# Kernel optimization log

Measured on AMD Instinct MI355X. Metric: run time of the kernel, lower is better.

The kernel has to match this reference:

```python
import jax, jax.numpy as jnp
import numpy as np

NUM_EXPERTS = 8
TOPK = 2
INPUT_DIM = 2048
OUTPUT_DIM = 2048


def setup_inputs() -> dict:
    key = jax.random.key(0)
    k_x, k_w, k_gw, k_gb = jax.random.split(key, 4)
    x = jax.random.normal(k_x, (8192, INPUT_DIM), dtype=jnp.float32)
    # experts: Linear(input_dim, output_dim*num_experts), xavier_uniform weight, zero bias
    fan_out = OUTPUT_DIM * NUM_EXPERTS
    limit = float(np.sqrt(6.0 / (INPUT_DIM + fan_out)))
    expert_w = jax.random.uniform(k_w, (fan_out, INPUT_DIM), minval=-limit, maxval=limit, dtype=jnp.float32)
    expert_b = jnp.zeros((fan_out,), dtype=jnp.float32)
    # gate: Linear(input_dim, num_experts), default torch init (uniform +-1/sqrt(fan_in))
    gl = 1.0 / float(np.sqrt(INPUT_DIM))
    gate_w = jax.random.uniform(k_gw, (NUM_EXPERTS, INPUT_DIM), minval=-gl, maxval=gl, dtype=jnp.float32)
    gate_b = jax.random.uniform(k_gb, (NUM_EXPERTS,), minval=-gl, maxval=gl, dtype=jnp.float32)
    return {"x": x, "expert_w": expert_w, "expert_b": expert_b, "gate_w": gate_w, "gate_b": gate_b}


def reference(x, expert_w, expert_b, gate_w, gate_b):
    B = x.shape[0]
    # gating
    gate_logits = x @ gate_w.T + gate_b                      # [B, E]
    gate_probs = jax.nn.softmax(gate_logits, axis=-1)
    top_k_probs, top_k_idx = jax.lax.top_k(gate_probs, TOPK)  # [B, K]
    # dense expert GEMM: all experts computed
    expert_out = x @ expert_w.T + expert_b                   # [B, E*D_out]
    expert_out = expert_out.reshape(B, NUM_EXPERTS, OUTPUT_DIM)
    # gather selected experts per token and combine
    sel = jnp.take_along_axis(expert_out, top_k_idx[:, :, None], axis=1)  # [B, K, D_out]
    out = jnp.sum(sel * top_k_probs[:, :, None], axis=1)     # [B, D_out]
    return out
```

## Files before the change

kernel.cpp:

```cpp
#include <hip/hip_runtime.h>

#define NUM_TOKENS 8192
#define DIM 2048
#define NE 8
#define BM 128
#define BN 128
#define BK 64

typedef __bf16 bf16x8 __attribute__((ext_vector_type(8)));
typedef float f32x4 __attribute__((ext_vector_type(4)));

typedef __attribute__((address_space(1))) const void* as1_cvp;
typedef __attribute__((address_space(3))) void* as3_vp;

__device__ __forceinline__ unsigned short f2bf(float f) {
  unsigned int u = __float_as_uint(f);
  unsigned int lsb = (u >> 16) & 1u;
  u += 0x7fffu + lsb;
  return (unsigned short)(u >> 16);
}
__device__ __forceinline__ float bflo(unsigned int u) {
  return __uint_as_float(u << 16);
}
__device__ __forceinline__ float bfhi(unsigned int u) {
  return __uint_as_float(u & 0xffff0000u);
}

__global__ __launch_bounds__(256) void convert_w_kernel(
    const float4* __restrict__ w, ushort4* __restrict__ wb) {
  int i = blockIdx.x * 256 + threadIdx.x;
  float4 v = w[i];
  ushort4 o;
  o.x = f2bf(v.x); o.y = f2bf(v.y); o.z = f2bf(v.z); o.w = f2bf(v.w);
  wb[i] = o;
}

__global__ __launch_bounds__(256) void gating_kernel(
    const float* __restrict__ x, const float* __restrict__ gw,
    const float* __restrict__ gb, unsigned short* __restrict__ xb,
    float* __restrict__ probs, int* __restrict__ routed) {
  const int wave = threadIdx.x >> 6;
  const int lane = threadIdx.x & 63;
  const int t = blockIdx.x * 4 + wave;
  const float4* xrow = (const float4*)(x + (size_t)t * DIM);
  ushort4* xbrow = (ushort4*)(xb + (size_t)t * DIM);
  float acc[NE];
#pragma unroll
  for (int e = 0; e < NE; ++e) acc[e] = 0.f;
#pragma unroll
  for (int it = 0; it < DIM / (4 * 64); ++it) {
    const int k4 = it * 64 + lane;
    float4 xv = xrow[k4];
    ushort4 o;
    o.x = f2bf(xv.x); o.y = f2bf(xv.y); o.z = f2bf(xv.z); o.w = f2bf(xv.w);
    xbrow[k4] = o;
#pragma unroll
    for (int e = 0; e < NE; ++e) {
      float4 wv = ((const float4*)(gw + (size_t)e * DIM))[k4];
      acc[e] += xv.x * wv.x + xv.y * wv.y + xv.z * wv.z + xv.w * wv.w;
    }
  }
#pragma unroll
  for (int e = 0; e < NE; ++e) {
#pragma unroll
    for (int off = 32; off > 0; off >>= 1)
      acc[e] += __shfl_xor(acc[e], off, 64);
  }
  if (lane == 0) {
    float p[NE];
    float mx = -1e30f;
#pragma unroll
    for (int e = 0; e < NE; ++e) {
      p[e] = acc[e] + gb[e];
      mx = fmaxf(mx, p[e]);
    }
    float s = 0.f;
#pragma unroll
    for (int e = 0; e < NE; ++e) { p[e] = __expf(p[e] - mx); s += p[e]; }
    float inv = 1.f / s;
#pragma unroll
    for (int e = 0; e < NE; ++e) p[e] *= inv;
    int e0 = 0;
#pragma unroll
    for (int e = 1; e < NE; ++e) if (p[e] > p[e0]) e0 = e;
    int e1 = (e0 == 0) ? 1 : 0;
#pragma unroll
    for (int e = 0; e < NE; ++e) if (e != e0 && p[e] > p[e1]) e1 = e;
    probs[t * 2 + 0] = p[e0];
    probs[t * 2 + 1] = p[e1];
    routed[t] = e0 | (e1 << 8);
  }
}

__global__ __launch_bounds__(256) void build_lists_kernel(
    const int* __restrict__ routed, int* __restrict__ lists,
    int* __restrict__ counts, int* __restrict__ tokpos) {
  const int e = blockIdx.x;
  const int tid = threadIdx.x;
  __shared__ int sc[256];
  __shared__ int sb[256];
  const int base_t = tid * (NUM_TOKENS / 256);
  int c = 0, cb = 0;
#pragma unroll 4
  for (int j = 0; j < NUM_TOKENS / 256; ++j) {
    int r = routed[base_t + j];
    int a0 = r & 0xff, a1 = (r >> 8) & 0xff;
    c += (a0 == e) + (a1 == e);
    cb += (a0 < e) + (a1 < e);
  }
  sc[tid] = c;
  sb[tid] = cb;
  __syncthreads();
  for (int ofs = 1; ofs < 256; ofs <<= 1) {
    int v = (tid >= ofs) ? sc[tid - ofs] : 0;
    int w = (tid >= ofs) ? sb[tid - ofs] : 0;
    __syncthreads();
    sc[tid] += v;
    sb[tid] += w;
    __syncthreads();
  }
  const int ebase = sb[255];
  int pos = sc[tid] - c;
#pragma unroll 4
  for (int j = 0; j < NUM_TOKENS / 256; ++j) {
    int t = base_t + j;
    int r = routed[t];
    if ((r & 0xff) == e) {
      lists[e * NUM_TOKENS + pos] = t;
      tokpos[2 * t] = ebase + pos;
      pos++;
    }
    if (((r >> 8) & 0xff) == e) {
      lists[e * NUM_TOKENS + pos] = t | 0x10000;
      tokpos[2 * t + 1] = ebase + pos;
      pos++;
    }
  }
  if (tid == 255) {
    counts[e] = sc[255];
    counts[8 + e] = ebase;
  }
}

__global__ __launch_bounds__(256) void moe_gemm_kernel(
    const unsigned short* __restrict__ xb,
    const unsigned short* __restrict__ wb,
    const float* __restrict__ eb,
    const float* __restrict__ probs,
    const int* __restrict__ lists,
    const int* __restrict__ counts,
    unsigned short* __restrict__ y,
    float* __restrict__ out,
    int use_y) {
  const int e = blockIdx.z;
  const int cnt = counts[e];
  const int s = blockIdx.x + 16 * blockIdx.y;
  const int xcd = s & 7;
  const int j = s >> 3;
  const int R = (j >> 4) * 8 + xcd;
  const int w4 = j & 15;
  const int mt = (R >> 2) * 4 + (w4 & 3);
  const int nt = (R & 3) * 4 + (w4 >> 2);
  const int m0 = mt * BM;
  if (m0 >= cnt) return;
  const int n0 = nt * BN;

  __shared__ __attribute__((aligned(16))) unsigned short As[BM * BK];
  __shared__ __attribute__((aligned(16))) unsigned short Bs[BN * BK];

  const int tid = threadIdx.x;
  const int wave = tid >> 6;
  const int lane = tid & 63;
  const int srow = lane >> 3;
  const int scol = ((lane & 7) ^ srow) * 8;

  const unsigned short* ag[4];
  const unsigned short* bg[4];
#pragma unroll
  for (int i = 0; i < 4; ++i) {
    int r = m0 + wave * 32 + i * 8 + srow;
    int rc = r < cnt ? r : cnt - 1;
    int tok = lists[e * NUM_TOKENS + rc] & 0xFFFF;
    ag[i] = xb + (size_t)tok * DIM + scol;
    int wr = e * DIM + n0 + wave * 32 + i * 8 + srow;
    bg[i] = wb + (size_t)wr * DIM + scol;
  }

  const f32x4 zero = {0.f, 0.f, 0.f, 0.f};
  f32x4 acc[4][4];
#pragma unroll
  for (int a = 0; a < 4; ++a)
#pragma unroll
    for (int b = 0; b < 4; ++b) acc[a][b] = zero;

  const int wm = (wave >> 1) * 64;
  const int wn = (wave & 1) * 64;
  const int frow = lane & 15;
  const int csel = lane >> 4;
  const int swz = lane & 7;

  for (int k0 = 0; k0 < DIM; k0 += BK) {
    __syncthreads();
#pragma unroll
    for (int i = 0; i < 4; ++i) {
      __builtin_amdgcn_global_load_lds(
          (as1_cvp)(ag[i] + k0),
          (as3_vp)(As + (wave * 32 + i * 8) * BK), 16, 0, 0);
      __builtin_amdgcn_global_load_lds(
          (as1_cvp)(bg[i] + k0),
          (as3_vp)(Bs + (wave * 32 + i * 8) * BK), 16, 0, 0);
    }
    __syncthreads();
#pragma unroll
    for (int kk = 0; kk < BK; kk += 32) {
      const int koff = ((((kk >> 3) | csel) ^ swz) << 3);
      bf16x8 af[4], bfr[4];
#pragma unroll
      for (int im = 0; im < 4; ++im)
        af[im] = *(const bf16x8*)(As + (wm + im * 16 + frow) * BK + koff);
#pragma unroll
      for (int in_ = 0; in_ < 4; ++in_)
        bfr[in_] = *(const bf16x8*)(Bs + (wn + in_ * 16 + frow) * BK + koff);
#pragma unroll
      for (int im = 0; im < 4; ++im)
#pragma unroll
        for (int in_ = 0; in_ < 4; ++in_)
          acc[im][in_] = __builtin_amdgcn_mfma_f32_16x16x32_bf16(
              af[im], bfr[in_], acc[im][in_], 0, 0, 0);
    }
  }

  const int quad = lane >> 4;
  const int col = lane & 15;
  const int ybase = counts[8 + e];
#pragma unroll
  for (int im = 0; im < 4; ++im) {
#pragma unroll
    for (int reg = 0; reg < 4; ++reg) {
      int r = m0 + wm + im * 16 + quad * 4 + reg;
      if (r >= cnt) continue;
      if (use_y) {
        unsigned short* yrow = y + (size_t)(ybase + r) * DIM;
#pragma unroll
        for (int in_ = 0; in_ < 4; ++in_) {
          int n = n0 + wn + in_ * 16 + col;
          yrow[n] = f2bf(acc[im][in_][reg] + eb[e * DIM + n]);
        }
      } else {
        int entry = lists[e * NUM_TOKENS + r];
        int tok = entry & 0xFFFF;
        int slot = entry >> 16;
        float p = probs[tok * 2 + slot];
        float* orow = out + (size_t)tok * DIM;
#pragma unroll
        for (int in_ = 0; in_ < 4; ++in_) {
          int n = n0 + wn + in_ * 16 + col;
          float v = acc[im][in_][reg] + eb[e * DIM + n];
          atomicAdd(orow + n, p * v);
        }
      }
    }
  }
}

__global__ __launch_bounds__(256) void combine_kernel(
    const unsigned short* __restrict__ y, const float* __restrict__ probs,
    const int* __restrict__ tokpos, float* __restrict__ out) {
  const int t = blockIdx.x;
  const int tid = threadIdx.x;
  const int i0 = tokpos[2 * t], i1 = tokpos[2 * t + 1];
  const float p0 = probs[2 * t], p1 = probs[2 * t + 1];
  uint4 a = ((const uint4*)(y + (size_t)i0 * DIM))[tid];
  uint4 b = ((const uint4*)(y + (size_t)i1 * DIM))[tid];
  float4 o0, o1;
  o0.x = p0 * bflo(a.x) + p1 * bflo(b.x);
  o0.y = p0 * bfhi(a.x) + p1 * bfhi(b.x);
  o0.z = p0 * bflo(a.y) + p1 * bflo(b.y);
  o0.w = p0 * bfhi(a.y) + p1 * bfhi(b.y);
  o1.x = p0 * bflo(a.z) + p1 * bflo(b.z);
  o1.y = p0 * bfhi(a.z) + p1 * bfhi(b.z);
  o1.z = p0 * bflo(a.w) + p1 * bflo(b.w);
  o1.w = p0 * bfhi(a.w) + p1 * bfhi(b.w);
  float4* orow = (float4*)(out + (size_t)t * DIM);
  orow[2 * tid] = o0;
  orow[2 * tid + 1] = o1;
}

extern "C" void kernel_launch(void* const* d_in, const int* in_sizes, int n_in,
                              void* d_out, int out_size, void* d_ws, size_t ws_size,
                              hipStream_t stream) {
  const float* x  = (const float*)d_in[0];
  const float* ew = (const float*)d_in[1];
  const float* eb = (const float*)d_in[2];
  const float* gw = (const float*)d_in[3];
  const float* gb = (const float*)d_in[4];
  float* out = (float*)d_out;
  char* p = (char*)d_ws;

  const size_t NEED = 67108864ull + 33554432ull + 67108864ull + 65536ull +
                      262144ull + 64ull + 32768ull + 65536ull;
  const int use_y = (ws_size >= NEED) ? 1 : 0;

  unsigned short* wb = (unsigned short*)p; p += 67108864;
  unsigned short* xb = (unsigned short*)p; p += 33554432;
  unsigned short* y = nullptr;
  if (use_y) { y = (unsigned short*)p; p += 67108864; }
  float* probs = (float*)p; p += 65536;
  int* lists   = (int*)p;   p += 262144;
  int* counts  = (int*)p;   p += 64;
  int* routed  = (int*)p;   p += 32768;
  int* tokpos  = (int*)p;   p += 65536;

  if (!use_y)
    hipMemsetAsync(out, 0, (size_t)NUM_TOKENS * DIM * sizeof(float), stream);
  convert_w_kernel<<<(NE * DIM * DIM / 4) / 256, 256, 0, stream>>>(
      (const float4*)ew, (ushort4*)wb);
  gating_kernel<<<NUM_TOKENS / 4, 256, 0, stream>>>(x, gw, gb, xb, probs,
                                                    routed);
  build_lists_kernel<<<NE, 256, 0, stream>>>(routed, lists, counts, tokpos);
  moe_gemm_kernel<<<dim3(DIM / BN, NUM_TOKENS / BM, NE), 256, 0, stream>>>(
      xb, wb, eb, probs, lists, counts, y, out, use_y);
  if (use_y)
    combine_kernel<<<NUM_TOKENS, 256, 0, stream>>>(y, probs, tokpos, out);
}
```

Before: 505.5 us.

## Enlarge MoE GEMM tiles to 256x256 with double-buffered LDS pipeline

Rewrites the grouped expert GEMM to use 256x256 tiles with 512 threads (8 waves, each computing 128x64), double-buffered LDS, and prefetch of the next K tile via direct global-to-LDS loads interleaved between MFMA phases. It also uses s_setprio around MFMA bursts and explicit vmcnt waits with raw barriers. The XCD-aware tile remapping is dropped in favour of plain block indexing. This is meant to raise arithmetic intensity and hide global-load latency, at the cost of 128 KB of LDS per block, more registers, and coarser tiles that waste more work on partially filled expert row tiles.

```diff
diff --git a/kernel.cpp b/kernel.cpp
--- a/kernel.cpp
+++ b/kernel.cpp
@@ -3,9 +3,10 @@
 #define NUM_TOKENS 8192
 #define DIM 2048
 #define NE 8
-#define BM 128
-#define BN 128
+#define BM 256
+#define BN 256
 #define BK 64
+#define KTILES (DIM / BK)
 
 typedef __bf16 bf16x8 __attribute__((ext_vector_type(8)));
 typedef float f32x4 __attribute__((ext_vector_type(4)));
@@ -25,6 +26,8 @@
 __device__ __forceinline__ float bfhi(unsigned int u) {
   return __uint_as_float(u & 0xffff0000u);
 }
+
+#define CFENCE() asm volatile("" ::: "memory")
 
 __global__ __launch_bounds__(256) void convert_w_kernel(
     const float4* __restrict__ w, ushort4* __restrict__ wb) {
@@ -142,7 +145,7 @@
   }
 }
 
-__global__ __launch_bounds__(256) void moe_gemm_kernel(
+__global__ __launch_bounds__(512, 2) void moe_gemm_kernel(
     const unsigned short* __restrict__ xb,
     const unsigned short* __restrict__ wb,
     const float* __restrict__ eb,
@@ -154,109 +157,171 @@
     int use_y) {
   const int e = blockIdx.z;
   const int cnt = counts[e];
-  const int s = blockIdx.x + 16 * blockIdx.y;
-  const int xcd = s & 7;
-  const int j = s >> 3;
-  const int R = (j >> 4) * 8 + xcd;
-  const int w4 = j & 15;
-  const int mt = (R >> 2) * 4 + (w4 & 3);
-  const int nt = (R & 3) * 4 + (w4 >> 2);
-  const int m0 = mt * BM;
+  const int m0 = blockIdx.y * BM;
   if (m0 >= cnt) return;
-  const int n0 = nt * BN;
-
-  __shared__ __attribute__((aligned(16))) unsigned short As[BM * BK];
-  __shared__ __attribute__((aligned(16))) unsigned short Bs[BN * BK];
+  const int n0 = blockIdx.x * BN;
+
+  __shared__ __attribute__((aligned(16))) unsigned short As[2][BM * BK];
+  __shared__ __attribute__((aligned(16))) unsigned short Bs[2][BN * BK];
 
   const int tid = threadIdx.x;
-  const int wave = tid >> 6;
-  const int lane = tid & 63;
-  const int srow = lane >> 3;
-  const int scol = ((lane & 7) ^ srow) * 8;
-
-  const unsigned short* ag[4];
-  const unsigned short* bg[4];
-#pragma unroll
-  for (int i = 0; i < 4; ++i) {
-    int r = m0 + wave * 32 + i * 8 + srow;
+  const int w = tid >> 6;
+  const int ln = tid & 63;
+  const int sr8 = ln >> 3;
+  const int sgc = ((ln & 7) ^ sr8) * 8;
+
+  const unsigned short* asrc[4];
+  const unsigned short* bsrc[4];
+#pragma unroll
+  for (int rb = 0; rb < 4; ++rb) {
+    int r = m0 + rb * 64 + w * 8 + sr8;
     int rc = r < cnt ? r : cnt - 1;
     int tok = lists[e * NUM_TOKENS + rc] & 0xFFFF;
-    ag[i] = xb + (size_t)tok * DIM + scol;
-    int wr = e * DIM + n0 + wave * 32 + i * 8 + srow;
-    bg[i] = wb + (size_t)wr * DIM + scol;
-  }
+    asrc[rb] = xb + (size_t)tok * DIM + sgc;
+    int wr = e * DIM + n0 + rb * 64 + w * 8 + sr8;
+    bsrc[rb] = wb + (size_t)wr * DIM + sgc;
+  }
+
+#define STAGE_A(buf, rb, k0)                                      \
+  __builtin_amdgcn_global_load_lds(                               \
+      (as1_cvp)(asrc[rb] + (k0)),                                 \
+      (as3_vp)(&As[buf][((rb)*64 + w * 8) * 64]), 16, 0, 0)
+#define STAGE_B(buf, rb, k0)                                      \
+  __builtin_amdgcn_global_load_lds(                               \
+      (as1_cvp)(bsrc[rb] + (k0)),                                 \
+      (as3_vp)(&Bs[buf][((rb)*64 + w * 8) * 64]), 16, 0, 0)
+
+#define BAR()            \
+  do {                   \
+    CFENCE();            \
+    __builtin_amdgcn_s_barrier(); \
+    CFENCE();            \
+  } while (0)
 
   const f32x4 zero = {0.f, 0.f, 0.f, 0.f};
-  f32x4 acc[4][4];
-#pragma unroll
-  for (int a = 0; a < 4; ++a)
+  f32x4 acc[8][4];
+#pragma unroll
+  for (int a = 0; a < 8; ++a)
 #pragma unroll
     for (int b = 0; b < 4; ++b) acc[a][b] = zero;
 
-  const int wm = (wave >> 1) * 64;
-  const int wn = (wave & 1) * 64;
-  const int frow = lane & 15;
-  const int csel = lane >> 4;
-  const int swz = lane & 7;
-
-  for (int k0 = 0; k0 < DIM; k0 += BK) {
-    __syncthreads();
+  const int wm = w >> 2;
+  const int wn = w & 3;
+  const int frow = ln & 15;
+  const int csel = ln >> 4;
+  const int f7 = frow & 7;
+  const int aro = (wm * 128 + frow) * 64;
+  const int bro = (wn * 64 + frow) * 64;
+  const int k0off = (csel ^ f7) * 8;
+  const int k1off = ((4 + csel) ^ f7) * 8;
+
+#pragma unroll
+  for (int rb = 0; rb < 4; ++rb) STAGE_A(0, rb, 0);
+#pragma unroll
+  for (int rb = 0; rb < 4; ++rb) STAGE_B(0, rb, 0);
+
+  for (int t = 0; t < KTILES; ++t) {
+    const int p = t & 1;
+    const int kn = (t + 1) * BK;
+    if (t + 1 < KTILES) {
+#pragma unroll
+      for (int rb = 0; rb < 4; ++rb) STAGE_A(p ^ 1, rb, kn);
+      asm volatile("s_waitcnt vmcnt(4)" ::: "memory");
+    } else {
+      asm volatile("s_waitcnt vmcnt(0)" ::: "memory");
+    }
+    BAR();
+    const unsigned short* Ap = As[p];
+    const unsigned short* Bp = Bs[p];
+    bf16x8 af[4], bf[4];
 #pragma unroll
     for (int i = 0; i < 4; ++i) {
-      __builtin_amdgcn_global_load_lds(
-          (as1_cvp)(ag[i] + k0),
-          (as3_vp)(As + (wave * 32 + i * 8) * BK), 16, 0, 0);
-      __builtin_amdgcn_global_load_lds(
-          (as1_cvp)(bg[i] + k0),
-          (as3_vp)(Bs + (wave * 32 + i * 8) * BK), 16, 0, 0);
-    }
-    __syncthreads();
-#pragma unroll
-    for (int kk = 0; kk < BK; kk += 32) {
-      const int koff = ((((kk >> 3) | csel) ^ swz) << 3);
-      bf16x8 af[4], bfr[4];
-#pragma unroll
-      for (int im = 0; im < 4; ++im)
-        af[im] = *(const bf16x8*)(As + (wm + im * 16 + frow) * BK + koff);
+      af[i] = *(const bf16x8*)(Ap + aro + i * 1024 + k0off);
+      bf[i] = *(const bf16x8*)(Bp + bro + i * 1024 + k0off);
+    }
+    __builtin_amdgcn_s_setprio(1);
+#pragma unroll
+    for (int im = 0; im < 4; ++im)
 #pragma unroll
       for (int in_ = 0; in_ < 4; ++in_)
-        bfr[in_] = *(const bf16x8*)(Bs + (wn + in_ * 16 + frow) * BK + koff);
-#pragma unroll
-      for (int im = 0; im < 4; ++im)
-#pragma unroll
-        for (int in_ = 0; in_ < 4; ++in_)
-          acc[im][in_] = __builtin_amdgcn_mfma_f32_16x16x32_bf16(
-              af[im], bfr[in_], acc[im][in_], 0, 0, 0);
-    }
-  }
-
-  const int quad = lane >> 4;
-  const int col = lane & 15;
+        acc[im][in_] = __builtin_amdgcn_mfma_f32_16x16x32_bf16(
+            af[im], bf[in_], acc[im][in_], 0, 0, 0);
+    __builtin_amdgcn_s_setprio(0);
+    BAR();
+#pragma unroll
+    for (int i = 0; i < 4; ++i)
+      af[i] = *(const bf16x8*)(Ap + aro + (i + 4) * 1024 + k0off);
+    if (t + 1 < KTILES) {
+#pragma unroll
+      for (int rb = 0; rb < 4; ++rb) STAGE_B(p ^ 1, rb, kn);
+    }
+    __builtin_amdgcn_s_setprio(1);
+#pragma unroll
+    for (int im = 0; im < 4; ++im)
+#pragma unroll
+      for (int in_ = 0; in_ < 4; ++in_)
+        acc[im + 4][in_] = __builtin_amdgcn_mfma_f32_16x16x32_bf16(
+            af[im], bf[in_], acc[im + 4][in_], 0, 0, 0);
+    __builtin_amdgcn_s_setprio(0);
+    BAR();
+#pragma unroll
+    for (int i = 0; i < 4; ++i) {
+      af[i] = *(const bf16x8*)(Ap + aro + i * 1024 + k1off);
+      bf[i] = *(const bf16x8*)(Bp + bro + i * 1024 + k1off);
+    }
+    __builtin_amdgcn_s_setprio(1);
+#pragma unroll
+    for (int im = 0; im < 4; ++im)
+#pragma unroll
+      for (int in_ = 0; in_ < 4; ++in_)
+        acc[im][in_] = __builtin_amdgcn_mfma_f32_16x16x32_bf16(
+            af[im], bf[in_], acc[im][in_], 0, 0, 0);
+    __builtin_amdgcn_s_setprio(0);
+    BAR();
+#pragma unroll
+    for (int i = 0; i < 4; ++i)
+      af[i] = *(const bf16x8*)(Ap + aro + (i + 4) * 1024 + k1off);
+    __builtin_amdgcn_s_setprio(1);
+#pragma unroll
+    for (int im = 0; im < 4; ++im)
+#pragma unroll
+      for (int in_ = 0; in_ < 4; ++in_)
+        acc[im + 4][in_] = __builtin_amdgcn_mfma_f32_16x16x32_bf16(
+            af[im], bf[in_], acc[im + 4][in_], 0, 0, 0);
+    __builtin_amdgcn_s_setprio(0);
+    BAR();
+  }
+#undef STAGE_A
+#undef STAGE_B
+#undef BAR
+
+  const int quad = ln >> 4;
+  const int col = ln & 15;
   const int ybase = counts[8 + e];
 #pragma unroll
-  for (int im = 0; im < 4; ++im) {
+  for (int im = 0; im < 8; ++im) {
 #pragma unroll
     for (int reg = 0; reg < 4; ++reg) {
-      int r = m0 + wm + im * 16 + quad * 4 + reg;
+      int r = m0 + wm * 128 + im * 16 + quad * 4 + reg;
       if (r >= cnt) continue;
       if (use_y) {
         unsigned short* yrow = y + (size_t)(ybase + r) * DIM;
 #pragma unroll
         for (int in_ = 0; in_ < 4; ++in_) {
-          int n = n0 + wn + in_ * 16 + col;
+          int n = n0 + wn * 64 + in_ * 16 + col;
           yrow[n] = f2bf(acc[im][in_][reg] + eb[e * DIM + n]);
         }
       } else {
         int entry = lists[e * NUM_TOKENS + r];
         int tok = entry & 0xFFFF;
         int slot = entry >> 16;
-        float p = probs[tok * 2 + slot];
+        float pw = probs[tok * 2 + slot];
         float* orow = out + (size_t)tok * DIM;
 #pragma unroll
         for (int in_ = 0; in_ < 4; ++in_) {
-          int n = n0 + wn + in_ * 16 + col;
+          int n = n0 + wn * 64 + in_ * 16 + col;
           float v = acc[im][in_][reg] + eb[e * DIM + n];
-          atomicAdd(orow + n, p * v);
+          atomicAdd(orow + n, pw * v);
         }
       }
     }
@@ -318,7 +383,7 @@
   gating_kernel<<<NUM_TOKENS / 4, 256, 0, stream>>>(x, gw, gb, xb, probs,
                                                     routed);
   build_lists_kernel<<<NE, 256, 0, stream>>>(routed, lists, counts, tokpos);
-  moe_gemm_kernel<<<dim3(DIM / BN, NUM_TOKENS / BM, NE), 256, 0, stream>>>(
+  moe_gemm_kernel<<<dim3(DIM / BN, NUM_TOKENS / BM, NE), 512, 0, stream>>>(
       xb, wb, eb, probs, lists, counts, y, out, use_y);
   if (use_y)
     combine_kernel<<<NUM_TOKENS, 256, 0, stream>>>(y, probs, tokpos, out);
```

New measurement: 513.2 us. Within noise of the previous version (+1.5%).

## Use persistent GEMM with atomic work queue over expert tiles

Applied to the files above, without the earlier changes.

Replaces the sparse 3D grid, where most blocks exit early because experts hold fewer tiles than the grid covers, with 768 persistent blocks. Each block pulls the next (expert, m-tile, n-tile) item from a global atomic counter. It also swaps the MFMA operand order so each lane holds 4 consecutive output columns, which allows vectorized bias loads and ushort4 stores to y. Launch bounds ask for 3 blocks per CU. The change loses the earlier XCD-aware tile ordering for L2 reuse and adds an atomic plus two barriers per tile.

```diff
diff --git a/kernel.cpp b/kernel.cpp
--- a/kernel.cpp
+++ b/kernel.cpp
@@ -6,6 +6,7 @@
 #define BM 128
 #define BN 128
 #define BK 64
+#define KTILES (DIM / BK)
 
 typedef __bf16 bf16x8 __attribute__((ext_vector_type(8)));
 typedef float f32x4 __attribute__((ext_vector_type(4)));
@@ -99,6 +100,7 @@
   const int tid = threadIdx.x;
   __shared__ int sc[256];
   __shared__ int sb[256];
+  if (e == 0 && tid == 0) counts[16] = 0;
   const int base_t = tid * (NUM_TOKENS / 256);
   int c = 0, cb = 0;
 #pragma unroll 4
@@ -142,121 +144,142 @@
   }
 }
 
-__global__ __launch_bounds__(256) void moe_gemm_kernel(
+__global__ __launch_bounds__(256, 3) void moe_gemm_kernel(
     const unsigned short* __restrict__ xb,
     const unsigned short* __restrict__ wb,
     const float* __restrict__ eb,
     const float* __restrict__ probs,
     const int* __restrict__ lists,
-    const int* __restrict__ counts,
+    int* __restrict__ counts,
     unsigned short* __restrict__ y,
     float* __restrict__ out,
     int use_y) {
-  const int e = blockIdx.z;
-  const int cnt = counts[e];
-  const int s = blockIdx.x + 16 * blockIdx.y;
-  const int xcd = s & 7;
-  const int j = s >> 3;
-  const int R = (j >> 4) * 8 + xcd;
-  const int w4 = j & 15;
-  const int mt = (R >> 2) * 4 + (w4 & 3);
-  const int nt = (R & 3) * 4 + (w4 >> 2);
-  const int m0 = mt * BM;
-  if (m0 >= cnt) return;
-  const int n0 = nt * BN;
-
   __shared__ __attribute__((aligned(16))) unsigned short As[BM * BK];
   __shared__ __attribute__((aligned(16))) unsigned short Bs[BN * BK];
+  __shared__ int s_w;
 
   const int tid = threadIdx.x;
-  const int wave = tid >> 6;
-  const int lane = tid & 63;
-  const int srow = lane >> 3;
-  const int scol = ((lane & 7) ^ srow) * 8;
-
-  const unsigned short* ag[4];
-  const unsigned short* bg[4];
-#pragma unroll
-  for (int i = 0; i < 4; ++i) {
-    int r = m0 + wave * 32 + i * 8 + srow;
-    int rc = r < cnt ? r : cnt - 1;
-    int tok = lists[e * NUM_TOKENS + rc] & 0xFFFF;
-    ag[i] = xb + (size_t)tok * DIM + scol;
-    int wr = e * DIM + n0 + wave * 32 + i * 8 + srow;
-    bg[i] = wb + (size_t)wr * DIM + scol;
-  }
-
-  const f32x4 zero = {0.f, 0.f, 0.f, 0.f};
-  f32x4 acc[4][4];
-#pragma unroll
-  for (int a = 0; a < 4; ++a)
-#pragma unroll
-    for (int b = 0; b < 4; ++b) acc[a][b] = zero;
-
-  const int wm = (wave >> 1) * 64;
-  const int wn = (wave & 1) * 64;
-  const int frow = lane & 15;
-  const int csel = lane >> 4;
-  const int swz = lane & 7;
-
-  for (int k0 = 0; k0 < DIM; k0 += BK) {
+  const int w = tid >> 6;
+  const int ln = tid & 63;
+  const int sr8 = ln >> 3;
+  const int sgc = ((ln & 7) ^ sr8) * 8;
+
+  int ntile[NE];
+  int wtot = 0;
+#pragma unroll
+  for (int i = 0; i < NE; ++i) {
+    ntile[i] = (counts[i] + BM - 1) >> 7;
+    wtot += ntile[i] << 4;
+  }
+
+  const int wm = (w >> 1) * 64;
+  const int wn = (w & 1) * 64;
+  const int frow = ln & 15;
+  const int csel = ln >> 4;
+  const int f7 = frow & 7;
+  const int k0off = (csel ^ f7) * 8;
+  const int k1off = ((4 + csel) ^ f7) * 8;
+  const int quad = ln >> 4;
+
+  for (;;) {
     __syncthreads();
+    if (tid == 0) s_w = atomicAdd(counts + 16, 1);
+    __syncthreads();
+    const int wi = s_w;
+    if (wi >= wtot) break;
+
+    int e = 0, rem = wi;
+    while (rem >= (ntile[e] << 4)) { rem -= ntile[e] << 4; ++e; }
+    const int mt = rem >> 4;
+    const int nt = rem & 15;
+    const int cnt = counts[e];
+    const int m0 = mt * BM;
+    const int n0 = nt * BN;
+
+    const unsigned short* asrc[4];
+    const unsigned short* bsrc[4];
 #pragma unroll
     for (int i = 0; i < 4; ++i) {
-      __builtin_amdgcn_global_load_lds(
-          (as1_cvp)(ag[i] + k0),
-          (as3_vp)(As + (wave * 32 + i * 8) * BK), 16, 0, 0);
-      __builtin_amdgcn_global_load_lds(
-          (as1_cvp)(bg[i] + k0),
-          (as3_vp)(Bs + (wave * 32 + i * 8) * BK), 16, 0, 0);
-    }
-    __syncthreads();
-#pragma unroll
-    for (int kk = 0; kk < BK; kk += 32) {
-      const int koff = ((((kk >> 3) | csel) ^ swz) << 3);
-      bf16x8 af[4], bfr[4];
-#pragma unroll
-      for (int im = 0; im < 4; ++im)
-        af[im] = *(const bf16x8*)(As + (wm + im * 16 + frow) * BK + koff);
-#pragma unroll
-      for (int in_ = 0; in_ < 4; ++in_)
-        bfr[in_] = *(const bf16x8*)(Bs + (wn + in_ * 16 + frow) * BK + koff);
-#pragma unroll
-      for (int im = 0; im < 4; ++im)
+      int r = m0 + w * 32 + i * 8 + sr8;
+      int rc = r < cnt ? r : cnt - 1;
+      int tok = lists[e * NUM_TOKENS + rc] & 0xFFFF;
+      asrc[i] = xb + (size_t)tok * DIM + sgc;
+      int wr = e * DIM + n0 + w * 32 + i * 8 + sr8;
+      bsrc[i] = wb + (size_t)wr * DIM + sgc;
+    }
+
+    const f32x4 zero = {0.f, 0.f, 0.f, 0.f};
+    f32x4 acc[4][4];
+#pragma unroll
+    for (int a = 0; a < 4; ++a)
+#pragma unroll
+      for (int b = 0; b < 4; ++b) acc[a][b] = zero;
+
+    for (int k0 = 0; k0 < DIM; k0 += BK) {
+      __syncthreads();
+#pragma unroll
+      for (int i = 0; i < 4; ++i) {
+        __builtin_amdgcn_global_load_lds(
+            (as1_cvp)(asrc[i] + k0),
+            (as3_vp)(As + (w * 32 + i * 8) * BK), 16, 0, 0);
+        __builtin_amdgcn_global_load_lds(
+            (as1_cvp)(bsrc[i] + k0),
+            (as3_vp)(Bs + (w * 32 + i * 8) * BK), 16, 0, 0);
+      }
+      __syncthreads();
+#pragma unroll
+      for (int kh = 0; kh < 2; ++kh) {
+        const int koff = kh ? k1off : k0off;
+        bf16x8 af[4], bfr[4];
+#pragma unroll
+        for (int im = 0; im < 4; ++im)
+          af[im] = *(const bf16x8*)(As + (wm + im * 16 + frow) * BK + koff);
 #pragma unroll
         for (int in_ = 0; in_ < 4; ++in_)
-          acc[im][in_] = __builtin_amdgcn_mfma_f32_16x16x32_bf16(
-              af[im], bfr[in_], acc[im][in_], 0, 0, 0);
-    }
-  }
-
-  const int quad = lane >> 4;
-  const int col = lane & 15;
-  const int ybase = counts[8 + e];
-#pragma unroll
-  for (int im = 0; im < 4; ++im) {
-#pragma unroll
-    for (int reg = 0; reg < 4; ++reg) {
-      int r = m0 + wm + im * 16 + quad * 4 + reg;
+          bfr[in_] = *(const bf16x8*)(Bs + (wn + in_ * 16 + frow) * BK + koff);
+#pragma unroll
+        for (int im = 0; im < 4; ++im)
+#pragma unroll
+          for (int in_ = 0; in_ < 4; ++in_)
+            acc[im][in_] = __builtin_amdgcn_mfma_f32_16x16x32_bf16(
+                bfr[in_], af[im], acc[im][in_], 0, 0, 0);
+      }
+    }
+
+    const int ybase = counts[8 + e];
+#pragma unroll
+    for (int im = 0; im < 4; ++im) {
+      int r = m0 + wm + im * 16 + frow;
       if (r >= cnt) continue;
       if (use_y) {
         unsigned short* yrow = y + (size_t)(ybase + r) * DIM;
 #pragma unroll
         for (int in_ = 0; in_ < 4; ++in_) {
-          int n = n0 + wn + in_ * 16 + col;
-          yrow[n] = f2bf(acc[im][in_][reg] + eb[e * DIM + n]);
+          int n = n0 + wn + in_ * 16 + quad * 4;
+          float4 ebv = *(const float4*)(eb + (size_t)e * DIM + n);
+          f32x4 v = acc[im][in_];
+          ushort4 o;
+          o.x = f2bf(v[0] + ebv.x);
+          o.y = f2bf(v[1] + ebv.y);
+          o.z = f2bf(v[2] + ebv.z);
+          o.w = f2bf(v[3] + ebv.w);
+          *(ushort4*)(yrow + n) = o;
         }
       } else {
         int entry = lists[e * NUM_TOKENS + r];
         int tok = entry & 0xFFFF;
         int slot = entry >> 16;
-        float p = probs[tok * 2 + slot];
+        float pw = probs[tok * 2 + slot];
         float* orow = out + (size_t)tok * DIM;
 #pragma unroll
         for (int in_ = 0; in_ < 4; ++in_) {
-          int n = n0 + wn + in_ * 16 + col;
-          float v = acc[im][in_][reg] + eb[e * DIM + n];
-          atomicAdd(orow + n, p * v);
+          int n = n0 + wn + in_ * 16 + quad * 4;
+          float4 ebv = *(const float4*)(eb + (size_t)e * DIM + n);
+          f32x4 v = acc[im][in_];
+          atomicAdd(orow + n + 0, pw * (v[0] + ebv.x));
+          atomicAdd(orow + n + 1, pw * (v[1] + ebv.y));
+          atomicAdd(orow + n + 2, pw * (v[2] + ebv.z));
+          atomicAdd(orow + n + 3, pw * (v[3] + ebv.w));
         }
       }
     }
@@ -298,7 +321,7 @@
   char* p = (char*)d_ws;
 
   const size_t NEED = 67108864ull + 33554432ull + 67108864ull + 65536ull +
-                      262144ull + 64ull + 32768ull + 65536ull;
+                      262144ull + 128ull + 32768ull + 65536ull;
   const int use_y = (ws_size >= NEED) ? 1 : 0;
 
   unsigned short* wb = (unsigned short*)p; p += 67108864;
@@ -307,7 +330,7 @@
   if (use_y) { y = (unsigned short*)p; p += 67108864; }
   float* probs = (float*)p; p += 65536;
   int* lists   = (int*)p;   p += 262144;
-  int* counts  = (int*)p;   p += 64;
+  int* counts  = (int*)p;   p += 128;
   int* routed  = (int*)p;   p += 32768;
   int* tokpos  = (int*)p;   p += 65536;
 
@@ -318,8 +341,8 @@
   gating_kernel<<<NUM_TOKENS / 4, 256, 0, stream>>>(x, gw, gb, xb, probs,
                                                     routed);
   build_lists_kernel<<<NE, 256, 0, stream>>>(routed, lists, counts, tokpos);
-  moe_gemm_kernel<<<dim3(DIM / BN, NUM_TOKENS / BM, NE), 256, 0, stream>>>(
-      xb, wb, eb, probs, lists, counts, y, out, use_y);
+  moe_gemm_kernel<<<768, 256, 0, stream>>>(xb, wb, eb, probs, lists, counts, y,
+                                           out, use_y);
   if (use_y)
     combine_kernel<<<NUM_TOKENS, 256, 0, stream>>>(y, probs, tokpos, out);
 }
```

Measured after the change: 572.6 us. 1.13x slower.
